# Kernel tuning notes

Measured on AMD Instinct MI355X. Metric: run time of the kernel, lower is better.

The kernel has to match this reference:

```python
import jax, jax.numpy as jnp
import numpy as np

NUM_HEADS = 8
NEG_SLOPE = 0.2
MASK_VAL = -10000000000.0


def setup_inputs() -> dict:
    key = jax.random.key(0)
    k1, k2, k3, k4 = jax.random.split(key, 4)
    B, N, H, d, T = 16, 256, NUM_HEADS, 64, 5
    src = jax.random.normal(k1, (B, N, H * d), dtype=jnp.float32)
    dst = jax.random.normal(k2, (B, N, H * d), dtype=jnp.float32)
    # parameter a: (atom_d*H, atom_d, T); xavier-ish scale
    a = jax.random.normal(k3, (H * d, d, T), dtype=jnp.float32) * 0.08
    # bond-type indices in [-1, T); -1 = no edge (masked)
    edges = jax.random.randint(k4, (B, N, N), -1, T, dtype=jnp.int64)
    return {"src_embeddings": src, "dst_embeddings": dst, "a": a, "edges": edges}


def reference(src_embeddings, dst_embeddings, a, edges):
    B, N, d_ = src_embeddings.shape
    H = NUM_HEADS
    d = d_ // H
    T = a.shape[-1]
    # (B, H, N, d)
    s = src_embeddings.reshape(B, N, H, d).transpose(0, 2, 1, 3)
    t = dst_embeddings.reshape(B, N, H, d).transpose(0, 2, 1, 3)
    # a.view(H, d, d*T) in torch == reshape(H, d, d, T) with (e, t) flattened
    A = a.reshape(H, d, d, T)
    # transformed_src[b,h,i,e,t] = sum_d s[b,h,i,d] * A[h,d,e,t]
    transformed = jnp.einsum('bhid,hdet->bhiet', s, A)
    # scores[b,h,i,j,t] = sum_e transformed[b,h,i,e,t] * t[b,h,j,e]  -> (B,H,N,N,T)
    scores = jnp.einsum('bhiet,bhje->bhijt', transformed, t)
    # gather the per-edge bond-type slice
    idx = jnp.broadcast_to(jnp.clip(edges, 0)[:, None, :, :, None], (B, H, N, N, 1))
    sel = jnp.take_along_axis(scores, idx, axis=-1)[..., 0]  # (B,H,N,N)
    mask = (edges == -1)[:, None, :, :]
    sel = jnp.where(mask, jnp.asarray(MASK_VAL, sel.dtype), sel)
    return jax.nn.leaky_relu(sel, negative_slope=NEG_SLOPE)
```

## Files before the change

kernel.cpp:

```cpp
#include <hip/hip_runtime.h>
#include <hip/hip_bf16.h>

#define NB 16
#define NN 256
#define NH 8
#define ND 64
#define NT 5
#define HD 512

typedef __bf16 bf16x8 __attribute__((ext_vector_type(8)));
typedef __bf16 bf16x4 __attribute__((ext_vector_type(4)));
typedef float  f32x4  __attribute__((ext_vector_type(4)));
typedef int    i32x4  __attribute__((ext_vector_type(4)));

__device__ __forceinline__ bf16x8 cvt8(f32x4 a, f32x4 b) {
    bf16x8 r;
    r[0] = (__bf16)a[0]; r[1] = (__bf16)a[1]; r[2] = (__bf16)a[2]; r[3] = (__bf16)a[3];
    r[4] = (__bf16)b[0]; r[5] = (__bf16)b[1]; r[6] = (__bf16)b[2]; r[7] = (__bf16)b[3];
    return r;
}

__device__ __forceinline__ void stage16(const void* g, void* l) {
    __builtin_amdgcn_global_load_lds(
        (const __attribute__((address_space(1))) void*)g,
        (__attribute__((address_space(3))) void*)l,
        16, 0, 0);
}

__global__ void prep_w_kernel(const float* __restrict__ a, __bf16* __restrict__ wt) {
    int idx = blockIdx.x * 256 + threadIdx.x;
    if (idx >= NH * ND * ND * NT) return;
    int t  = idx % NT;
    int e  = (idx / NT) % ND;
    int dd = (idx / (NT * ND)) % ND;
    int h  = idx / (NT * ND * ND);
    wt[(((h * NT + t) * ND + e) * ND) + dd] = (__bf16)a[idx];
}

#define LW   0
#define LS0  40960
#define LS1  45056
#define LS2  0
#define LE0  49152
#define LE1  53248
#define LE2  4096
#define LP0  8192
#define LP1  18432

__global__ __launch_bounds__(256, 2) void mhea_fused(
    const float* __restrict__ src, const float* __restrict__ dst,
    const __bf16* __restrict__ wt, const int* __restrict__ edges,
    float* __restrict__ out)
{
    __shared__ alignas(16) unsigned char Lb[57344];

    const int bid = blockIdx.x;
    const int wg  = (bid & 7) * 64 + (bid >> 3);
    const int b   = wg >> 5;
    const int h   = (wg >> 2) & 7;
    const int jq  = wg & 3;
    const int j0  = jq * 64;

    const int tid = threadIdx.x;
    const int w   = tid >> 6;
    const int l   = tid & 63;
    const int il  = l & 15;
    const int kg  = l >> 4;

    const int SOFF[3] = {LS0, LS1, LS2};
    const int EOFF[3] = {LE0, LE1, LE2};
    const int POFF[2] = {LP0, LP1};

    bf16x8 cb0, cb1;
    {
        const float* dp = dst + ((size_t)(b * NN + j0 + w * 16 + il)) * HD + h * ND;
        f32x4 q0 = *reinterpret_cast<const f32x4*>(dp + kg * 8);
        f32x4 q1 = *reinterpret_cast<const f32x4*>(dp + kg * 8 + 4);
        f32x4 q2 = *reinterpret_cast<const f32x4*>(dp + 32 + kg * 8);
        f32x4 q3 = *reinterpret_cast<const f32x4*>(dp + 36 + kg * 8);
        cb0 = cvt8(q0, q1);
        cb1 = cvt8(q2, q3);
    }

    {
        const __bf16* wbase = wt + (size_t)(h * NT) * ND * ND;
        __bf16* Wl = (__bf16*)(Lb + LW);
        #pragma unroll
        for (int k = 0; k < 10; ++k) {
            const int idx = w * 10 + k;
            const int t   = idx >> 3;
            const int sub = idx & 7;
            const int e   = sub * 8 + (l >> 3);
            const int c   = (l & 7) ^ (e & 7);
            stage16(wbase + ((size_t)t * ND + e) * ND + c * 8,
                    Wl + t * 4096 + sub * 512);
        }
    }
    #pragma unroll
    for (int p = 0; p < 2; ++p) {
        const int row = w * 4 + (l >> 4);
        const int c   = (l & 15) ^ (row & 7);
        stage16(src + ((size_t)(b * NN + p * 16 + row)) * HD + h * ND + c * 4,
                Lb + SOFF[p] + w * 1024);
        stage16(edges + ((size_t)(b * NN + p * 16 + row)) * NN + j0 + c * 4,
                Lb + EOFF[p] + w * 1024);
    }

    asm volatile("s_waitcnt vmcnt(0)" ::: "memory");
    __builtin_amdgcn_sched_barrier(0);
    __builtin_amdgcn_s_barrier();

    bf16x8 wa[NT][2];
    {
        const __bf16* Wl = (const __bf16*)(Lb + LW);
        #pragma unroll
        for (int t = 0; t < NT; ++t)
            #pragma unroll
            for (int ks = 0; ks < 2; ++ks)
                wa[t][ks] = *reinterpret_cast<const bf16x8*>(
                    Wl + t * 4096 + (w * 16 + il) * ND + (((ks * 4 + kg) ^ (il & 7)) << 3));
    }
    asm volatile("s_waitcnt lgkmcnt(0)" ::: "memory");
    __builtin_amdgcn_sched_barrier(0);
    __builtin_amdgcn_s_barrier();

    #pragma unroll
    for (int k = 0; k < 16; ++k) {
        const float* Sc = (const float*)(Lb + SOFF[k % 3]);
        const int*   Ec = (const int*)  (Lb + EOFF[k % 3]);
        __bf16*      Pc = (__bf16*)     (Lb + POFF[k & 1]);

        if (k < 14) {
            const int i2  = (k + 2) * 16;
            const int row = w * 4 + (l >> 4);
            const int c   = (l & 15) ^ (row & 7);
            stage16(src + ((size_t)(b * NN + i2 + row)) * HD + h * ND + c * 4,
                    Lb + SOFF[(k + 2) % 3] + w * 1024);
            stage16(edges + ((size_t)(b * NN + i2 + row)) * NN + j0 + c * 4,
                    Lb + EOFF[(k + 2) % 3] + w * 1024);
        }

        const i32x4 ce = *reinterpret_cast<const i32x4*>(
            Ec + il * 64 + (((w * 4 + kg) ^ (il & 7)) << 2));

        {
            f32x4 a0 = *reinterpret_cast<const f32x4*>(&Sc[il * ND + (((2 * kg + 0) ^ (il & 7)) << 2)]);
            f32x4 a1 = *reinterpret_cast<const f32x4*>(&Sc[il * ND + (((2 * kg + 1) ^ (il & 7)) << 2)]);
            f32x4 a2 = *reinterpret_cast<const f32x4*>(&Sc[il * ND + (((8 + 2 * kg) ^ (il & 7)) << 2)]);
            f32x4 a3 = *reinterpret_cast<const f32x4*>(&Sc[il * ND + (((9 + 2 * kg) ^ (il & 7)) << 2)]);
            bf16x8 bf0 = cvt8(a0, a1);
            bf16x8 bf1 = cvt8(a2, a3);
            #pragma unroll
            for (int t = 0; t < NT; ++t) {
                f32x4 pacc = {0.f, 0.f, 0.f, 0.f};
                pacc = __builtin_amdgcn_mfma_f32_16x16x32_bf16(wa[t][0], bf0, pacc, 0, 0, 0);
                pacc = __builtin_amdgcn_mfma_f32_16x16x32_bf16(wa[t][1], bf1, pacc, 0, 0, 0);
                bf16x4 pk;
                pk[0] = (__bf16)pacc[0];
                pk[1] = (__bf16)pacc[1];
                pk[2] = (__bf16)pacc[2];
                pk[3] = (__bf16)pacc[3];
                const int elem = (w * 16 + kg * 4) ^ ((il & 7) << 3);
                *reinterpret_cast<bf16x4*>(Pc + t * 1024 + il * ND + elem) = pk;
            }
        }

        if (k < 14) {
            asm volatile("s_waitcnt vmcnt(3) lgkmcnt(0)" ::: "memory");
        } else {
            asm volatile("s_waitcnt vmcnt(1) lgkmcnt(0)" ::: "memory");
        }
        __builtin_amdgcn_sched_barrier(0);
        __builtin_amdgcn_s_barrier();

        {
            bf16x8 pa[NT][2];
            #pragma unroll
            for (int t = 0; t < NT; ++t)
                #pragma unroll
                for (int ks = 0; ks < 2; ++ks)
                    pa[t][ks] = *reinterpret_cast<const bf16x8*>(
                        Pc + t * 1024 + il * ND + (((ks * 4 + kg) ^ (il & 7)) << 3));

            f32x4 acc[NT];
            #pragma unroll
            for (int t = 0; t < NT; ++t) {
                acc[t] = (f32x4){0.f, 0.f, 0.f, 0.f};
                acc[t] = __builtin_amdgcn_mfma_f32_16x16x32_bf16(cb0, pa[t][0], acc[t], 0, 0, 0);
                acc[t] = __builtin_amdgcn_mfma_f32_16x16x32_bf16(cb1, pa[t][1], acc[t], 0, 0, 0);
            }

            f32x4 o;
            #pragma unroll
            for (int r = 0; r < 4; ++r) {
                const int ev = ce[r];
                float x;
                if (ev < 0) { x = -1e10f; }
                else {
                    x = (ev == 0) ? acc[0][r]
                      : (ev == 1) ? acc[1][r]
                      : (ev == 2) ? acc[2][r]
                      : (ev == 3) ? acc[3][r]
                      :             acc[4][r];
                }
                o[r] = (x >= 0.f) ? x : 0.2f * x;
            }
            *reinterpret_cast<f32x4*>(
                out + ((size_t)(b * NH + h) * NN + k * 16 + il) * NN
                    + j0 + w * 16 + kg * 4) = o;
        }
    }
}

__global__ __launch_bounds__(64, 3) void mhea_fused_fallback(
    const float* __restrict__ src, const float* __restrict__ dst,
    const float* __restrict__ araw, const int* __restrict__ edges,
    float* __restrict__ out)
{
    __shared__ __bf16 Plds[NT * 16 * 64];

    const int it = blockIdx.x;
    const int h  = blockIdx.y;
    const int b  = blockIdx.z;
    const int i0 = it * 16;

    const int l  = threadIdx.x & 63;
    const int il = l & 15;
    const int kg = l >> 4;

    const float* dbase = dst + (size_t)b * NN * HD + h * ND;
    const int*   erow  = edges + ((size_t)b * NN + i0 + il) * NN;
    const float* sbase = src + (size_t)(b * NN + i0 + il) * HD + h * ND;

    f32x4 s0 = *reinterpret_cast<const f32x4*>(sbase + kg * 8);
    f32x4 s1 = *reinterpret_cast<const f32x4*>(sbase + kg * 8 + 4);
    f32x4 s2 = *reinterpret_cast<const f32x4*>(sbase + 32 + kg * 8);
    f32x4 s3 = *reinterpret_cast<const f32x4*>(sbase + 36 + kg * 8);
    bf16x8 af0 = cvt8(s0, s1);
    bf16x8 af1 = cvt8(s2, s3);

    #pragma unroll
    for (int t = 0; t < NT; ++t) {
        #pragma unroll
        for (int et = 0; et < 4; ++et) {
            bf16x8 w0, w1;
            #pragma unroll
            for (int jj = 0; jj < 8; ++jj) {
                const int ee = et * 16 + il;
                w0[jj] = (__bf16)araw[((size_t)(h * ND + kg * 8 + jj) * ND + ee) * NT + t];
                w1[jj] = (__bf16)araw[((size_t)(h * ND + kg * 8 + jj + 32) * ND + ee) * NT + t];
            }
            f32x4 pacc = {0.f, 0.f, 0.f, 0.f};
            pacc = __builtin_amdgcn_mfma_f32_16x16x32_bf16(w0, af0, pacc, 0, 0, 0);
            pacc = __builtin_amdgcn_mfma_f32_16x16x32_bf16(w1, af1, pacc, 0, 0, 0);
            bf16x4 pk;
            pk[0] = (__bf16)pacc[0];
            pk[1] = (__bf16)pacc[1];
            pk[2] = (__bf16)pacc[2];
            pk[3] = (__bf16)pacc[3];
            const int elem = (et * 16 + kg * 4) ^ ((il & 7) << 3);
            *reinterpret_cast<bf16x4*>(&Plds[t * 1024 + il * 64 + elem]) = pk;
        }
    }

    bf16x8 pa[NT][2];
    #pragma unroll
    for (int t = 0; t < NT; ++t) {
        #pragma unroll
        for (int ks = 0; ks < 2; ++ks) {
            const int elem = (ks * 32 + kg * 8) ^ ((il & 7) << 3);
            pa[t][ks] = *reinterpret_cast<const bf16x8*>(&Plds[t * 1024 + il * 64 + elem]);
        }
    }

    float* obase = out + (((size_t)(b * NH + h)) * NN + i0 + il) * NN;

    for (int jt = 0; jt < 16; ++jt) {
        const float* np = dbase + (size_t)(jt * 16 + il) * HD + kg * 8;
        f32x4 d0 = *reinterpret_cast<const f32x4*>(np);
        f32x4 d1 = *reinterpret_cast<const f32x4*>(np + 4);
        f32x4 d2 = *reinterpret_cast<const f32x4*>(np + 32);
        f32x4 d3 = *reinterpret_cast<const f32x4*>(np + 36);
        i32x4 ce = *reinterpret_cast<const i32x4*>(erow + jt * 16 + kg * 4);
        const bf16x8 cb0 = cvt8(d0, d1);
        const bf16x8 cb1 = cvt8(d2, d3);
        f32x4 acc[NT];
        #pragma unroll
        for (int t = 0; t < NT; ++t) {
            acc[t] = (f32x4){0.f, 0.f, 0.f, 0.f};
            acc[t] = __builtin_amdgcn_mfma_f32_16x16x32_bf16(cb0, pa[t][0], acc[t], 0, 0, 0);
            acc[t] = __builtin_amdgcn_mfma_f32_16x16x32_bf16(cb1, pa[t][1], acc[t], 0, 0, 0);
        }
        f32x4 o;
        #pragma unroll
        for (int r = 0; r < 4; ++r) {
            const int ev = ce[r];
            float x;
            if (ev < 0) { x = -1e10f; }
            else {
                x = (ev == 0) ? acc[0][r]
                  : (ev == 1) ? acc[1][r]
                  : (ev == 2) ? acc[2][r]
                  : (ev == 3) ? acc[3][r]
                  :             acc[4][r];
            }
            o[r] = (x >= 0.f) ? x : 0.2f * x;
        }
        *reinterpret_cast<f32x4*>(obase + jt * 16 + kg * 4) = o;
    }
}

extern "C" void kernel_launch(void* const* d_in, const int* in_sizes, int n_in,
                              void* d_out, int out_size, void* d_ws, size_t ws_size,
                              hipStream_t stream) {
    const float* src   = (const float*)d_in[0];
    const float* dst   = (const float*)d_in[1];
    const float* a     = (const float*)d_in[2];
    const int*   edges = (const int*)d_in[3];
    float* out = (float*)d_out;

    const size_t wt_bytes = (size_t)NH * NT * ND * ND * sizeof(__bf16);

    if (ws_size >= wt_bytes) {
        __bf16* wt = (__bf16*)d_ws;
        const int total = NH * ND * ND * NT;
        prep_w_kernel<<<(total + 255) / 256, 256, 0, stream>>>(a, wt);
        mhea_fused<<<512, 256, 0, stream>>>(src, dst, wt, edges, out);
    } else {
        mhea_fused_fallback<<<dim3(NN / 16, NH, NB), 64, 0, stream>>>(
            src, dst, a, edges, out);
    }
}
```

Before: 32.84 us.

## Retile fused kernel to 128x128 blocks with 8 waves splitting the transform GEMM

Each block now covers 128 source rows by 128 destination columns using 512 threads, instead of all 256 rows by 64 columns using 256 threads. The first GEMM (source times the per-bond-type weights) is split across 8 waves: 4 e-slices times 2 groups of bond types. Previously 4 blocks per (batch, head) each recomputed the transform for all rows; now that redundant work is halved. The LDS layout is reshuffled so the P buffers reuse the weight region once the weights sit in registers, and s_setprio is raised around the MFMA sections. The cost is a larger 64 KB LDS footprint, uneven bond-type work between the two wave groups, and fewer pipeline iterations over which to hide load latency.

```diff
diff --git a/kernel.cpp b/kernel.cpp
--- a/kernel.cpp
+++ b/kernel.cpp
@@ -38,28 +38,30 @@
 }
 
 #define LW   0
+#define LP0  0
+#define LP1  10240
+#define LS2  20480
+#define LE2  24576
 #define LS0  40960
 #define LS1  45056
-#define LS2  0
 #define LE0  49152
-#define LE1  53248
-#define LE2  4096
-#define LP0  8192
-#define LP1  18432
-
-__global__ __launch_bounds__(256, 2) void mhea_fused(
+#define LE1  57344
+
+__global__ __launch_bounds__(512, 2) void mhea_fused(
     const float* __restrict__ src, const float* __restrict__ dst,
     const __bf16* __restrict__ wt, const int* __restrict__ edges,
     float* __restrict__ out)
 {
-    __shared__ alignas(16) unsigned char Lb[57344];
+    __shared__ alignas(16) unsigned char Lb[65536];
 
     const int bid = blockIdx.x;
     const int wg  = (bid & 7) * 64 + (bid >> 3);
     const int b   = wg >> 5;
     const int h   = (wg >> 2) & 7;
-    const int jq  = wg & 3;
-    const int j0  = jq * 64;
+    const int jh  = (wg >> 1) & 1;
+    const int ih  = wg & 1;
+    const int j0  = jh * 128;
+    const int ib0 = ih * 128;
 
     const int tid = threadIdx.x;
     const int w   = tid >> 6;
@@ -67,9 +69,13 @@
     const int il  = l & 15;
     const int kg  = l >> 4;
 
-    const int SOFF[3] = {LS0, LS1, LS2};
-    const int EOFF[3] = {LE0, LE1, LE2};
-    const int POFF[2] = {LP0, LP1};
+    const int et  = w & 3;
+    const int tl  = w >> 2;
+    const int t0  = tl * 3;
+    const int ntl = 3 - tl;
+
+    const int SO[3] = {LS0, LS1, LS2};
+    const int EO[3] = {LE0, LE1, LE2};
 
     bf16x8 cb0, cb1;
     {
@@ -84,64 +90,78 @@
 
     {
         const __bf16* wbase = wt + (size_t)(h * NT) * ND * ND;
-        __bf16* Wl = (__bf16*)(Lb + LW);
-        #pragma unroll
-        for (int k = 0; k < 10; ++k) {
-            const int idx = w * 10 + k;
+        #pragma unroll
+        for (int k = 0; k < 5; ++k) {
+            const int idx = w * 5 + k;
             const int t   = idx >> 3;
             const int sub = idx & 7;
             const int e   = sub * 8 + (l >> 3);
             const int c   = (l & 7) ^ (e & 7);
             stage16(wbase + ((size_t)t * ND + e) * ND + c * 8,
-                    Wl + t * 4096 + sub * 512);
+                    Lb + LW + t * 8192 + sub * 1024);
+        }
+    }
+    if (w < 4) {
+        #pragma unroll
+        for (int p = 0; p < 2; ++p) {
+            const int row = w * 4 + (l >> 4);
+            const int c   = (l & 15) ^ (row & 7);
+            stage16(src + ((size_t)(b * NN + ib0 + p * 16 + row)) * HD + h * ND + c * 4,
+                    Lb + SO[p] + w * 1024);
         }
     }
     #pragma unroll
     for (int p = 0; p < 2; ++p) {
-        const int row = w * 4 + (l >> 4);
-        const int c   = (l & 15) ^ (row & 7);
-        stage16(src + ((size_t)(b * NN + p * 16 + row)) * HD + h * ND + c * 4,
-                Lb + SOFF[p] + w * 1024);
-        stage16(edges + ((size_t)(b * NN + p * 16 + row)) * NN + j0 + c * 4,
-                Lb + EOFF[p] + w * 1024);
+        const int row = w * 2 + (l >> 5);
+        const int c   = (l & 31) ^ (row & 7);
+        stage16(edges + ((size_t)(b * NN + ib0 + p * 16 + row)) * NN + j0 + c * 4,
+                Lb + EO[p] + w * 1024);
     }
 
     asm volatile("s_waitcnt vmcnt(0)" ::: "memory");
     __builtin_amdgcn_sched_barrier(0);
     __builtin_amdgcn_s_barrier();
 
-    bf16x8 wa[NT][2];
-    {
-        const __bf16* Wl = (const __bf16*)(Lb + LW);
-        #pragma unroll
-        for (int t = 0; t < NT; ++t)
+    bf16x8 wa[3][2];
+    #pragma unroll
+    for (int tt = 0; tt < 3; ++tt) {
+        if (tt < ntl) {
+            const int t = t0 + tt;
             #pragma unroll
             for (int ks = 0; ks < 2; ++ks)
-                wa[t][ks] = *reinterpret_cast<const bf16x8*>(
-                    Wl + t * 4096 + (w * 16 + il) * ND + (((ks * 4 + kg) ^ (il & 7)) << 3));
+                wa[tt][ks] = *reinterpret_cast<const bf16x8*>(
+                    Lb + LW + t * 8192 + (et * 16 + il) * 128
+                       + (((ks * 4 + kg) ^ (il & 7)) << 4));
+        }
     }
     asm volatile("s_waitcnt lgkmcnt(0)" ::: "memory");
     __builtin_amdgcn_sched_barrier(0);
     __builtin_amdgcn_s_barrier();
 
     #pragma unroll
-    for (int k = 0; k < 16; ++k) {
-        const float* Sc = (const float*)(Lb + SOFF[k % 3]);
-        const int*   Ec = (const int*)  (Lb + EOFF[k % 3]);
-        __bf16*      Pc = (__bf16*)     (Lb + POFF[k & 1]);
-
-        if (k < 14) {
-            const int i2  = (k + 2) * 16;
-            const int row = w * 4 + (l >> 4);
-            const int c   = (l & 15) ^ (row & 7);
-            stage16(src + ((size_t)(b * NN + i2 + row)) * HD + h * ND + c * 4,
-                    Lb + SOFF[(k + 2) % 3] + w * 1024);
-            stage16(edges + ((size_t)(b * NN + i2 + row)) * NN + j0 + c * 4,
-                    Lb + EOFF[(k + 2) % 3] + w * 1024);
+    for (int k = 0; k < 8; ++k) {
+        const float* Sc = (const float*)(Lb + SO[k % 3]);
+        const int*   Ec = (const int*)  (Lb + EO[k % 3]);
+        __bf16*      Pc = (__bf16*)     (Lb + ((k & 1) ? LP1 : LP0));
+
+        if (k < 6) {
+            const int i2 = ib0 + (k + 2) * 16;
+            if (w < 4) {
+                const int row = w * 4 + (l >> 4);
+                const int c   = (l & 15) ^ (row & 7);
+                stage16(src + ((size_t)(b * NN + i2 + row)) * HD + h * ND + c * 4,
+                        Lb + SO[(k + 2) % 3] + w * 1024);
+            }
+            {
+                const int row = w * 2 + (l >> 5);
+                const int c   = (l & 31) ^ (row & 7);
+                stage16(edges + ((size_t)(b * NN + i2 + row)) * NN + j0 + c * 4,
+                        Lb + EO[(k + 2) % 3] + w * 1024);
+            }
         }
 
         const i32x4 ce = *reinterpret_cast<const i32x4*>(
-            Ec + il * 64 + (((w * 4 + kg) ^ (il & 7)) << 2));
+            Ec + il * 128 + (((w * 4 + kg) ^ (il & 7)) << 2));
 
         {
             f32x4 a0 = *reinterpret_cast<const f32x4*>(&Sc[il * ND + (((2 * kg + 0) ^ (il & 7)) << 2)]);
@@ -150,23 +170,29 @@
             f32x4 a3 = *reinterpret_cast<const f32x4*>(&Sc[il * ND + (((9 + 2 * kg) ^ (il & 7)) << 2)]);
             bf16x8 bf0 = cvt8(a0, a1);
             bf16x8 bf1 = cvt8(a2, a3);
-            #pragma unroll
-            for (int t = 0; t < NT; ++t) {
-                f32x4 pacc = {0.f, 0.f, 0.f, 0.f};
-                pacc = __builtin_amdgcn_mfma_f32_16x16x32_bf16(wa[t][0], bf0, pacc, 0, 0, 0);
-                pacc = __builtin_amdgcn_mfma_f32_16x16x32_bf16(wa[t][1], bf1, pacc, 0, 0, 0);
-                bf16x4 pk;
-                pk[0] = (__bf16)pacc[0];
-                pk[1] = (__bf16)pacc[1];
-                pk[2] = (__bf16)pacc[2];
-                pk[3] = (__bf16)pacc[3];
-                const int elem = (w * 16 + kg * 4) ^ ((il & 7) << 3);
-                *reinterpret_cast<bf16x4*>(Pc + t * 1024 + il * ND + elem) = pk;
-            }
-        }
-
-        if (k < 14) {
-            asm volatile("s_waitcnt vmcnt(3) lgkmcnt(0)" ::: "memory");
+            __builtin_amdgcn_s_setprio(1);
+            #pragma unroll
+            for (int tt = 0; tt < 3; ++tt) {
+                if (tt < ntl) {
+                    const int t = t0 + tt;
+                    f32x4 pacc = {0.f, 0.f, 0.f, 0.f};
+                    pacc = __builtin_amdgcn_mfma_f32_16x16x32_bf16(wa[tt][0], bf0, pacc, 0, 0, 0);
+                    pacc = __builtin_amdgcn_mfma_f32_16x16x32_bf16(wa[tt][1], bf1, pacc, 0, 0, 0);
+                    bf16x4 pk;
+                    pk[0] = (__bf16)pacc[0];
+                    pk[1] = (__bf16)pacc[1];
+                    pk[2] = (__bf16)pacc[2];
+                    pk[3] = (__bf16)pacc[3];
+                    const int elem = (et * 16 + kg * 4) ^ ((il & 7) << 3);
+                    *reinterpret_cast<bf16x4*>(Pc + t * 1024 + il * ND + elem) = pk;
+                }
+            }
+            __builtin_amdgcn_s_setprio(0);
+        }
+
+        if (k < 6) {
+            if (w < 4) { asm volatile("s_waitcnt vmcnt(3) lgkmcnt(0)" ::: "memory"); }
+            else       { asm volatile("s_waitcnt vmcnt(2) lgkmcnt(0)" ::: "memory"); }
         } else {
             asm volatile("s_waitcnt vmcnt(1) lgkmcnt(0)" ::: "memory");
         }
@@ -182,6 +208,7 @@
                     pa[t][ks] = *reinterpret_cast<const bf16x8*>(
                         Pc + t * 1024 + il * ND + (((ks * 4 + kg) ^ (il & 7)) << 3));
 
+            __builtin_amdgcn_s_setprio(1);
             f32x4 acc[NT];
             #pragma unroll
             for (int t = 0; t < NT; ++t) {
@@ -189,6 +216,7 @@
                 acc[t] = __builtin_amdgcn_mfma_f32_16x16x32_bf16(cb0, pa[t][0], acc[t], 0, 0, 0);
                 acc[t] = __builtin_amdgcn_mfma_f32_16x16x32_bf16(cb1, pa[t][1], acc[t], 0, 0, 0);
             }
+            __builtin_amdgcn_s_setprio(0);
 
             f32x4 o;
             #pragma unroll
@@ -206,7 +234,7 @@
                 o[r] = (x >= 0.f) ? x : 0.2f * x;
             }
             *reinterpret_cast<f32x4*>(
-                out + ((size_t)(b * NH + h) * NN + k * 16 + il) * NN
+                out + ((size_t)(b * NH + h) * NN + ib0 + k * 16 + il) * NN
                     + j0 + w * 16 + kg * 4) = o;
         }
     }
@@ -325,7 +353,7 @@
         __bf16* wt = (__bf16*)d_ws;
         const int total = NH * ND * ND * NT;
         prep_w_kernel<<<(total + 255) / 256, 256, 0, stream>>>(a, wt);
-        mhea_fused<<<512, 256, 0, stream>>>(src, dst, wt, edges, out);
+        mhea_fused<<<512, 512, 0, stream>>>(src, dst, wt, edges, out);
     } else {
         mhea_fused_fallback<<<dim3(NN / 16, NH, NB), 64, 0, stream>>>(
             src, dst, a, edges, out);
```

New measurement: 27.50 us. 16.3% less time.

## Split i dimension across 4x more workgroups and drop per-row pipeline

Applied to the files above, without the earlier changes.

The fused kernel now launches 2048 workgroups, each handling a 64x64 (i,j) tile instead of a full 256-row strip. All src and edge tiles are staged up front, the first-stage projections for all four row blocks are computed before a single barrier, and the per-step triple-buffered pipeline with its 16 barriers is removed. Weights are read straight from global into registers instead of going through LDS. The weight prep kernel writes 8 bf16 per thread with vector stores. The aim is more parallelism and fewer barriers, at the cost of 73 KB of LDS per block, which caps occupancy, and of reloading weights and dst once per i-tile.

```diff
diff --git a/kernel.cpp b/kernel.cpp
--- a/kernel.cpp
+++ b/kernel.cpp
@@ -28,48 +28,42 @@
 }
 
 __global__ void prep_w_kernel(const float* __restrict__ a, __bf16* __restrict__ wt) {
-    int idx = blockIdx.x * 256 + threadIdx.x;
-    if (idx >= NH * ND * ND * NT) return;
-    int t  = idx % NT;
-    int e  = (idx / NT) % ND;
-    int dd = (idx / (NT * ND)) % ND;
-    int h  = idx / (NT * ND * ND);
-    wt[(((h * NT + t) * ND + e) * ND) + dd] = (__bf16)a[idx];
-}
-
-#define LW   0
-#define LS0  40960
-#define LS1  45056
-#define LS2  0
-#define LE0  49152
-#define LE1  53248
-#define LE2  4096
-#define LP0  8192
-#define LP1  18432
+    const int o8 = (blockIdx.x * 256 + threadIdx.x) * 8;
+    if (o8 >= NH * ND * ND * NT) return;
+    const int dd0 = o8 & 63;
+    const int e   = (o8 >> 6) & 63;
+    const int ht  = o8 >> 12;
+    const int t   = ht % NT;
+    const int h   = ht / NT;
+    bf16x8 v;
+    #pragma unroll
+    for (int j = 0; j < 8; ++j)
+        v[j] = (__bf16)a[((size_t)(h * ND + dd0 + j) * ND + e) * NT + t];
+    *reinterpret_cast<bf16x8*>(wt + o8) = v;
+}
 
 __global__ __launch_bounds__(256, 2) void mhea_fused(
     const float* __restrict__ src, const float* __restrict__ dst,
     const __bf16* __restrict__ wt, const int* __restrict__ edges,
     float* __restrict__ out)
 {
-    __shared__ alignas(16) unsigned char Lb[57344];
+    __shared__ alignas(16) unsigned char Lb[73728];
 
     const int bid = blockIdx.x;
-    const int wg  = (bid & 7) * 64 + (bid >> 3);
-    const int b   = wg >> 5;
-    const int h   = (wg >> 2) & 7;
-    const int jq  = wg & 3;
+    const int wg  = (bid & 7) * 256 + (bid >> 3);
+    const int b   = wg >> 7;
+    const int rem = wg & 127;
+    const int h   = rem >> 4;
+    const int jq  = (rem >> 2) & 3;
+    const int iq  = rem & 3;
     const int j0  = jq * 64;
+    const int i0  = iq * 64;
 
     const int tid = threadIdx.x;
     const int w   = tid >> 6;
     const int l   = tid & 63;
     const int il  = l & 15;
     const int kg  = l >> 4;
-
-    const int SOFF[3] = {LS0, LS1, LS2};
-    const int EOFF[3] = {LE0, LE1, LE2};
-    const int POFF[2] = {LP0, LP1};
 
     bf16x8 cb0, cb1;
     {
@@ -81,134 +75,98 @@
         cb0 = cvt8(q0, q1);
         cb1 = cvt8(q2, q3);
     }
+    bf16x8 wa[NT][2];
+    #pragma unroll
+    for (int t = 0; t < NT; ++t)
+        #pragma unroll
+        for (int ks = 0; ks < 2; ++ks)
+            wa[t][ks] = *reinterpret_cast<const bf16x8*>(
+                wt + (((size_t)(h * NT + t) * ND) + w * 16 + il) * ND + ks * 32 + kg * 8);
 
     {
-        const __bf16* wbase = wt + (size_t)(h * NT) * ND * ND;
-        __bf16* Wl = (__bf16*)(Lb + LW);
-        #pragma unroll
-        for (int k = 0; k < 10; ++k) {
-            const int idx = w * 10 + k;
-            const int t   = idx >> 3;
-            const int sub = idx & 7;
-            const int e   = sub * 8 + (l >> 3);
-            const int c   = (l & 7) ^ (e & 7);
-            stage16(wbase + ((size_t)t * ND + e) * ND + c * 8,
-                    Wl + t * 4096 + sub * 512);
-        }
-    }
-    #pragma unroll
-    for (int p = 0; p < 2; ++p) {
         const int row = w * 4 + (l >> 4);
         const int c   = (l & 15) ^ (row & 7);
-        stage16(src + ((size_t)(b * NN + p * 16 + row)) * HD + h * ND + c * 4,
-                Lb + SOFF[p] + w * 1024);
-        stage16(edges + ((size_t)(b * NN + p * 16 + row)) * NN + j0 + c * 4,
-                Lb + EOFF[p] + w * 1024);
-    }
-
-    asm volatile("s_waitcnt vmcnt(0)" ::: "memory");
+        #pragma unroll
+        for (int it = 0; it < 4; ++it)
+            stage16(src + ((size_t)(b * NN + i0 + it * 16 + row)) * HD + h * ND + c * 4,
+                    Lb + it * 4096 + w * 1024);
+        #pragma unroll
+        for (int it = 0; it < 4; ++it)
+            stage16(edges + ((size_t)(b * NN + i0 + it * 16 + row)) * NN + j0 + c * 4,
+                    Lb + 16384 + it * 4096 + w * 1024);
+    }
+
+    asm volatile("s_waitcnt vmcnt(4)" ::: "memory");
     __builtin_amdgcn_sched_barrier(0);
     __builtin_amdgcn_s_barrier();
 
-    bf16x8 wa[NT][2];
-    {
-        const __bf16* Wl = (const __bf16*)(Lb + LW);
-        #pragma unroll
-        for (int t = 0; t < NT; ++t)
-            #pragma unroll
-            for (int ks = 0; ks < 2; ++ks)
-                wa[t][ks] = *reinterpret_cast<const bf16x8*>(
-                    Wl + t * 4096 + (w * 16 + il) * ND + (((ks * 4 + kg) ^ (il & 7)) << 3));
-    }
-    asm volatile("s_waitcnt lgkmcnt(0)" ::: "memory");
+    #pragma unroll
+    for (int it = 0; it < 4; ++it) {
+        const float* Sc = (const float*)(Lb + it * 4096);
+        __bf16*      Pc = (__bf16*)(Lb + 32768 + it * 10240);
+        f32x4 a0 = *reinterpret_cast<const f32x4*>(&Sc[il * ND + (((2 * kg + 0) ^ (il & 7)) << 2)]);
+        f32x4 a1 = *reinterpret_cast<const f32x4*>(&Sc[il * ND + (((2 * kg + 1) ^ (il & 7)) << 2)]);
+        f32x4 a2 = *reinterpret_cast<const f32x4*>(&Sc[il * ND + (((8 + 2 * kg) ^ (il & 7)) << 2)]);
+        f32x4 a3 = *reinterpret_cast<const f32x4*>(&Sc[il * ND + (((9 + 2 * kg) ^ (il & 7)) << 2)]);
+        bf16x8 bf0 = cvt8(a0, a1);
+        bf16x8 bf1 = cvt8(a2, a3);
+        #pragma unroll
+        for (int t = 0; t < NT; ++t) {
+            f32x4 pacc = {0.f, 0.f, 0.f, 0.f};
+            pacc = __builtin_amdgcn_mfma_f32_16x16x32_bf16(wa[t][0], bf0, pacc, 0, 0, 0);
+            pacc = __builtin_amdgcn_mfma_f32_16x16x32_bf16(wa[t][1], bf1, pacc, 0, 0, 0);
+            bf16x4 pk;
+            pk[0] = (__bf16)pacc[0];
+            pk[1] = (__bf16)pacc[1];
+            pk[2] = (__bf16)pacc[2];
+            pk[3] = (__bf16)pacc[3];
+            const int elem = (w * 16 + kg * 4) ^ ((il & 7) << 3);
+            *reinterpret_cast<bf16x4*>(Pc + t * 1024 + il * ND + elem) = pk;
+        }
+    }
+
+    asm volatile("s_waitcnt vmcnt(0) lgkmcnt(0)" ::: "memory");
     __builtin_amdgcn_sched_barrier(0);
     __builtin_amdgcn_s_barrier();
 
     #pragma unroll
-    for (int k = 0; k < 16; ++k) {
-        const float* Sc = (const float*)(Lb + SOFF[k % 3]);
-        const int*   Ec = (const int*)  (Lb + EOFF[k % 3]);
-        __bf16*      Pc = (__bf16*)     (Lb + POFF[k & 1]);
-
-        if (k < 14) {
-            const int i2  = (k + 2) * 16;
-            const int row = w * 4 + (l >> 4);
-            const int c   = (l & 15) ^ (row & 7);
-            stage16(src + ((size_t)(b * NN + i2 + row)) * HD + h * ND + c * 4,
-                    Lb + SOFF[(k + 2) % 3] + w * 1024);
-            stage16(edges + ((size_t)(b * NN + i2 + row)) * NN + j0 + c * 4,
-                    Lb + EOFF[(k + 2) % 3] + w * 1024);
-        }
+    for (int it = 0; it < 4; ++it) {
+        const __bf16* Pc = (const __bf16*)(Lb + 32768 + it * 10240);
+        const int*    Ec = (const int*)(Lb + 16384 + it * 4096);
 
         const i32x4 ce = *reinterpret_cast<const i32x4*>(
             Ec + il * 64 + (((w * 4 + kg) ^ (il & 7)) << 2));
 
-        {
-            f32x4 a0 = *reinterpret_cast<const f32x4*>(&Sc[il * ND + (((2 * kg + 0) ^ (il & 7)) << 2)]);
-            f32x4 a1 = *reinterpret_cast<const f32x4*>(&Sc[il * ND + (((2 * kg + 1) ^ (il & 7)) << 2)]);
-            f32x4 a2 = *reinterpret_cast<const f32x4*>(&Sc[il * ND + (((8 + 2 * kg) ^ (il & 7)) << 2)]);
-            f32x4 a3 = *reinterpret_cast<const f32x4*>(&Sc[il * ND + (((9 + 2 * kg) ^ (il & 7)) << 2)]);
-            bf16x8 bf0 = cvt8(a0, a1);
-            bf16x8 bf1 = cvt8(a2, a3);
-            #pragma unroll
-            for (int t = 0; t < NT; ++t) {
-                f32x4 pacc = {0.f, 0.f, 0.f, 0.f};
-                pacc = __builtin_amdgcn_mfma_f32_16x16x32_bf16(wa[t][0], bf0, pacc, 0, 0, 0);
-                pacc = __builtin_amdgcn_mfma_f32_16x16x32_bf16(wa[t][1], bf1, pacc, 0, 0, 0);
-                bf16x4 pk;
-                pk[0] = (__bf16)pacc[0];
-                pk[1] = (__bf16)pacc[1];
-                pk[2] = (__bf16)pacc[2];
-                pk[3] = (__bf16)pacc[3];
-                const int elem = (w * 16 + kg * 4) ^ ((il & 7) << 3);
-                *reinterpret_cast<bf16x4*>(Pc + t * 1024 + il * ND + elem) = pk;
+        f32x4 acc[NT];
+        #pragma unroll
+        for (int t = 0; t < NT; ++t) {
+            const bf16x8 pa0 = *reinterpret_cast<const bf16x8*>(
+                Pc + t * 1024 + il * ND + (((0 * 4 + kg) ^ (il & 7)) << 3));
+            const bf16x8 pa1 = *reinterpret_cast<const bf16x8*>(
+                Pc + t * 1024 + il * ND + (((1 * 4 + kg) ^ (il & 7)) << 3));
+            acc[t] = (f32x4){0.f, 0.f, 0.f, 0.f};
+            acc[t] = __builtin_amdgcn_mfma_f32_16x16x32_bf16(cb0, pa0, acc[t], 0, 0, 0);
+            acc[t] = __builtin_amdgcn_mfma_f32_16x16x32_bf16(cb1, pa1, acc[t], 0, 0, 0);
+        }
+
+        f32x4 o;
+        #pragma unroll
+        for (int r = 0; r < 4; ++r) {
+            const int ev = ce[r];
+            float x;
+            if (ev < 0) { x = -1e10f; }
+            else {
+                x = (ev == 0) ? acc[0][r]
+                  : (ev == 1) ? acc[1][r]
+                  : (ev == 2) ? acc[2][r]
+                  : (ev == 3) ? acc[3][r]
+                  :             acc[4][r];
             }
-        }
-
-        if (k < 14) {
-            asm volatile("s_waitcnt vmcnt(3) lgkmcnt(0)" ::: "memory");
-        } else {
-            asm volatile("s_waitcnt vmcnt(1) lgkmcnt(0)" ::: "memory");
-        }
-        __builtin_amdgcn_sched_barrier(0);
-        __builtin_amdgcn_s_barrier();
-
-        {
-            bf16x8 pa[NT][2];
-            #pragma unroll
-            for (int t = 0; t < NT; ++t)
-                #pragma unroll
-                for (int ks = 0; ks < 2; ++ks)
-                    pa[t][ks] = *reinterpret_cast<const bf16x8*>(
-                        Pc + t * 1024 + il * ND + (((ks * 4 + kg) ^ (il & 7)) << 3));
-
-            f32x4 acc[NT];
-            #pragma unroll
-            for (int t = 0; t < NT; ++t) {
-                acc[t] = (f32x4){0.f, 0.f, 0.f, 0.f};
-                acc[t] = __builtin_amdgcn_mfma_f32_16x16x32_bf16(cb0, pa[t][0], acc[t], 0, 0, 0);
-                acc[t] = __builtin_amdgcn_mfma_f32_16x16x32_bf16(cb1, pa[t][1], acc[t], 0, 0, 0);
-            }
-
-            f32x4 o;
-            #pragma unroll
-            for (int r = 0; r < 4; ++r) {
-                const int ev = ce[r];
-                float x;
-                if (ev < 0) { x = -1e10f; }
-                else {
-                    x = (ev == 0) ? acc[0][r]
-                      : (ev == 1) ? acc[1][r]
-                      : (ev == 2) ? acc[2][r]
-                      : (ev == 3) ? acc[3][r]
-                      :             acc[4][r];
-                }
-                o[r] = (x >= 0.f) ? x : 0.2f * x;
-            }
-            *reinterpret_cast<f32x4*>(
-                out + ((size_t)(b * NH + h) * NN + k * 16 + il) * NN
-                    + j0 + w * 16 + kg * 4) = o;
-        }
+            o[r] = (x >= 0.f) ? x : 0.2f * x;
+        }
+        *reinterpret_cast<f32x4*>(
+            out + ((size_t)(b * NH + h) * NN + i0 + it * 16 + il) * NN
+                + j0 + w * 16 + kg * 4) = o;
     }
 }
 
@@ -324,8 +282,8 @@
     if (ws_size >= wt_bytes) {
         __bf16* wt = (__bf16*)d_ws;
         const int total = NH * ND * ND * NT;
-        prep_w_kernel<<<(total + 255) / 256, 256, 0, stream>>>(a, wt);
-        mhea_fused<<<512, 256, 0, stream>>>(src, dst, wt, edges, out);
+        prep_w_kernel<<<(total / 8 + 255) / 256, 256, 0, stream>>>(a, wt);
+        mhea_fused<<<2048, 256, 0, stream>>>(src, dst, wt, edges, out);
     } else {
         mhea_fused_fallback<<<dim3(NN / 16, NH, NB), 64, 0, stream>>>(
             src, dst, a, edges, out);
```

New measurement: 37.66 us. 14.7% more time.
